# Performance work log

Measured on AMD Instinct MI355X. Metric: run time of the kernel, lower is better.

## Reference

```python
import jax, jax.numpy as jnp
import numpy as np


def _conv(x, w, stride):
    # Conv2d(k=3, stride, padding=1, bias=False), NCHW/OIHW
    return jax.lax.conv_general_dilated(
        x, w, (stride, stride), ((1, 1), (1, 1)),
        dimension_numbers=('NCHW', 'OIHW', 'NCHW'))


def _bn_silu(x, g, b, m, v):
    # BatchNorm2d (inference) + SiLU, fused elementwise
    scale = (g * jax.lax.rsqrt(v + 1e-5))[None, :, None, None]
    y = (x - m[None, :, None, None]) * scale + b[None, :, None, None]
    return y * jax.nn.sigmoid(y)


def _ss2d(x, in_w, dt_w, dt_b, B_w, C_w, A_log, D, out_w):
    # Low-rank 2D selective scan over flattened spatial tokens.
    Bn, C, H, W = x.shape
    L = H * W
    xt = x.reshape(Bn, C, L).transpose(0, 2, 1)            # [B,L,C]
    u = jnp.einsum('blc,rc->blr', xt, in_w)                # low-rank input [B,L,R]
    dt = jax.nn.softplus(jnp.einsum('blc,rc->blr', xt, dt_w) + dt_b)
    Bt = jnp.einsum('blc,nc->bln', xt, B_w)                # [B,L,N]
    Ct = jnp.einsum('blc,nc->bln', xt, C_w)                # [B,L,N]
    A = -jnp.exp(A_log)                                    # [R,N], stable (negative)

    def step(h, inp):
        u_t, dt_t, b_t, c_t = inp                          # [B,R],[B,R],[B,N],[B,N]
        dA = jnp.exp(dt_t[..., None] * A)                  # [B,R,N]
        h = dA * h + (dt_t[..., None] * b_t[:, None, :]) * u_t[..., None]
        y = jnp.einsum('brn,bn->br', h, c_t)               # [B,R]
        return h, (h, y)

    R, N = A_log.shape
    h0 = jnp.zeros((Bn, R, N), x.dtype)
    xs = (u.transpose(1, 0, 2), dt.transpose(1, 0, 2),
          Bt.transpose(1, 0, 2), Ct.transpose(1, 0, 2))
    _, (hs, ys) = jax.lax.scan(step, h0, xs)               # hs:[L,B,R,N] ys:[L,B,R]
    y = ys.transpose(1, 0, 2) + D * u                      # skip term D*u
    out = jnp.einsum('blr,cr->blc', y, out_w)              # project back to C
    x_out = (xt + out).transpose(0, 2, 1).reshape(Bn, C, H, W)
    state_seq = hs.transpose(1, 0, 2, 3)                   # [B,L,R,N]
    return x_out, state_seq


def setup_inputs() -> dict:
    key = jax.random.key(0)
    ks = jax.random.split(key, 24)
    f = jax.random.normal
    B, Cin, H, W = 8, 32, 112, 112
    E, R, N, NB = 64, 32, 64, 3
    inp = {}
    inp['x'] = f(ks[0], (B, Cin, H, W), jnp.float32)
    # stem
    inp['stem_w'] = f(ks[1], (E, Cin, 3, 3)) * 0.05
    inp['stem_g'] = 1.0 + 0.1 * f(ks[2], (E,))
    inp['stem_b'] = 0.1 * f(ks[3], (E,))
    inp['stem_m'] = 0.1 * f(ks[4], (E,))
    inp['stem_v'] = 1.0 + 0.1 * jax.random.uniform(ks[5], (E,))
    # SS2D blocks (stacked over num_blocks)
    inp['blk_in_w'] = f(ks[6], (NB, R, E)) * 0.1
    inp['blk_dt_w'] = f(ks[7], (NB, R, E)) * 0.05
    inp['blk_dt_b'] = f(ks[8], (NB, R)) * 0.1 - 2.0
    inp['blk_B_w'] = f(ks[9], (NB, N, E)) * 0.1
    inp['blk_C_w'] = f(ks[10], (NB, N, E)) * 0.1
    inp['blk_A_log'] = jnp.log(1.0 + jax.random.uniform(ks[11], (NB, R, N)) * 4.0)
    inp['blk_D'] = f(ks[12], (NB, R)) * 0.1
    inp['blk_out_w'] = f(ks[13], (NB, E, R)) * 0.1
    # down p4
    C4, C5 = 2 * E, 4 * E
    inp['p4_w'] = f(ks[14], (C4, E, 3, 3)) * 0.05
    inp['p4_g'] = 1.0 + 0.1 * f(ks[15], (C4,))
    inp['p4_b'] = 0.1 * f(ks[16], (C4,))
    inp['p4_m'] = 0.1 * f(ks[17], (C4,))
    inp['p4_v'] = 1.0 + 0.1 * jax.random.uniform(ks[18], (C4,))
    # down p5
    inp['p5_w'] = f(ks[19], (C5, C4, 3, 3)) * 0.05
    inp['p5_g'] = 1.0 + 0.1 * f(ks[20], (C5,))
    inp['p5_b'] = 0.1 * f(ks[21], (C5,))
    inp['p5_m'] = 0.1 * f(ks[22], (C5,))
    inp['p5_v'] = 1.0 + 0.1 * jax.random.uniform(ks[23], (C5,))
    return inp


def reference(x, stem_w, stem_g, stem_b, stem_m, stem_v,
              blk_in_w, blk_dt_w, blk_dt_b, blk_B_w, blk_C_w,
              blk_A_log, blk_D, blk_out_w,
              p4_w, p4_g, p4_b, p4_m, p4_v,
              p5_w, p5_g, p5_b, p5_m, p5_v):
    x = _bn_silu(_conv(x, stem_w, 2), stem_g, stem_b, stem_m, stem_v)
    states = []
    for i in range(blk_in_w.shape[0]):
        x, s = _ss2d(x, blk_in_w[i], blk_dt_w[i], blk_dt_b[i],
                     blk_B_w[i], blk_C_w[i], blk_A_log[i], blk_D[i], blk_out_w[i])
        states.append(s)
    p3 = x
    p4 = _bn_silu(_conv(p3, p4_w, 2), p4_g, p4_b, p4_m, p4_v)
    p5 = _bn_silu(_conv(p4, p5_w, 2), p5_g, p5_b, p5_m, p5_v)
    return (p3, p4, p5, jnp.stack(states))
```

## Files before the change

kernel.cpp:

```cpp
#include <hip/hip_runtime.h>
#include <cstdint>
#include <cstddef>

#define RFL(x) __builtin_amdgcn_readfirstlane(x)

constexpr int E  = 64;
constexpr int Rr = 32;
constexpr int Nn = 64;
constexpr int Lt = 3136;
constexpr int NC = 28;
constexpr int CL = 112;
constexpr int PD = 192;

__global__ __launch_bounds__(256) void k_wtrans(const float* __restrict__ in_w,
    const float* __restrict__ dt_w, const float* __restrict__ B_w,
    const float* __restrict__ C_w, float* __restrict__ wT) {
  int idx = blockIdx.x * 256 + threadIdx.x;
  if (idx >= 3 * 64 * PD) return;
  int o = idx % PD; int c = (idx / PD) & 63; int i = idx / (PD * 64);
  float v;
  if (o < 32)       v = in_w[(i * 32 + o) * 64 + c];
  else if (o < 64)  v = dt_w[(i * 32 + (o - 32)) * 64 + c];
  else if (o < 128) v = B_w[(i * 64 + (o - 64)) * 64 + c];
  else              v = C_w[(i * 64 + (o - 128)) * 64 + c];
  wT[idx] = v;
}

__global__ __launch_bounds__(256) void k_cwt2(const float* __restrict__ w,
    float* __restrict__ w3, int Cout, int Cin) {
  int idx = blockIdx.x * 256 + threadIdx.x;
  if (idx >= Cin * Cout * 9) return;
  int co = idx % Cout; int k = (idx / Cout) % 9; int ci = idx / (9 * Cout);
  w3[idx] = w[((size_t)co * Cin + ci) * 9 + k];
}

template<int CIN, int COUT, int HIN, int WIN>
__global__ __launch_bounds__(256) void k_conv(const float* __restrict__ x,
    const float* __restrict__ w3, const float* __restrict__ g, const float* __restrict__ bb,
    const float* __restrict__ m, const float* __restrict__ vv, float* __restrict__ out) {
  constexpr int HOUT = HIN / 2, WOUT = WIN / 2;
  constexpr int OWT = 7;
  constexpr int GWX = WOUT / OWT;
  constexpr int CIW = CIN / 4;
  __shared__ float xs[3][CIN][16];
  __shared__ float tbuf[4][64][8];

  int t = blockIdx.x;
  int b = t & 7; t >>= 3;
  int oh = t % HOUT; t /= HOUT;
  int gx = t % GWX; int cog = t / GWX;
  int lane = threadIdx.x & 63;
  int ws = RFL(threadIdx.x >> 6);
  int co = cog * 64 + lane;
  int iwb = gx * 14;
  int ih0 = oh * 2 - 1;

  for (int i = threadIdx.x; i < CIN * 3 * 16; i += 256) {
    int d = i & 15; int r3 = i >> 4;
    int kh = r3 / CIN; int ci = r3 & (CIN - 1);
    int iw = iwb + d - 1; int ih = ih0 + kh;
    float v = 0.f;
    if ((unsigned)iw < (unsigned)WIN && (unsigned)ih < (unsigned)HIN)
      v = x[(((size_t)(b * CIN + ci)) * HIN + ih) * WIN + iw];
    xs[kh][ci][d] = v;
  }
  __syncthreads();

  float acc[OWT];
#pragma unroll
  for (int o = 0; o < OWT; ++o) acc[o] = 0.f;

  int ci0 = ws * CIW;
#pragma unroll 2
  for (int cc = 0; cc < CIW; ++cc) {
    int ci = ci0 + cc;
    const float* wr = w3 + ((size_t)ci * 9) * COUT + co;
    float wk[9];
#pragma unroll
    for (int k = 0; k < 9; ++k) wk[k] = wr[(size_t)k * COUT];
#pragma unroll
    for (int kh = 0; kh < 3; ++kh) {
      const float4* tp4 = (const float4*)(&xs[kh][ci][0]);
      float4 q0 = tp4[0], q1 = tp4[1], q2 = tp4[2], q3 = tp4[3];
      float tp[16] = {q0.x, q0.y, q0.z, q0.w, q1.x, q1.y, q1.z, q1.w,
                      q2.x, q2.y, q2.z, q2.w, q3.x, q3.y, q3.z, q3.w};
#pragma unroll
      for (int o = 0; o < OWT; ++o) {
        acc[o] = fmaf(tp[2*o],     wk[kh*3+0], acc[o]);
        acc[o] = fmaf(tp[2*o + 1], wk[kh*3+1], acc[o]);
        acc[o] = fmaf(tp[2*o + 2], wk[kh*3+2], acc[o]);
      }
    }
  }
#pragma unroll
  for (int o = 0; o < OWT; ++o) tbuf[ws][lane][o] = acc[o];
  __syncthreads();

  for (int i = threadIdx.x; i < 64 * OWT; i += 256) {
    int cl = i / OWT, o = i - cl * OWT;
    float s = tbuf[0][cl][o] + tbuf[1][cl][o] + tbuf[2][cl][o] + tbuf[3][cl][o];
    int c2 = cog * 64 + cl;
    float scale = g[c2] * rsqrtf(vv[c2] + 1e-5f);
    float yv = (s - m[c2]) * scale + bb[c2];
    out[(((size_t)(b * COUT + c2)) * HOUT + oh) * WOUT + gx * OWT + o] =
        yv / (1.f + __expf(-yv));
  }
}

__global__ __launch_bounds__(256) void k_proj(const float* __restrict__ xin,
    const float* __restrict__ wT, const float* __restrict__ dt_b, float* __restrict__ P) {
  __shared__ float sm[64 * 196];
  int b = blockIdx.x & 7, tl = blockIdx.x >> 3;
  int l0 = tl * 64;
  int tid = threadIdx.x;
  for (int k = 0; k < 16; ++k) {
    int idx = k * 256 + tid; int c = idx >> 6, li = idx & 63;
    sm[c * 65 + li] = xin[(size_t)(b * 64 + c) * Lt + l0 + li];
  }
  __syncthreads();
  int tok = tid & 63;
  int og = RFL(tid >> 6);
  const float* wbase = wT + og * 48;
  float acc[48];
#pragma unroll
  for (int j = 0; j < 48; ++j) acc[j] = 0.f;
  for (int c = 0; c < 64; ++c) {
    float xv = sm[c * 65 + tok];
    const float4* w4 = (const float4*)(wbase + c * PD);
#pragma unroll
    for (int j = 0; j < 12; ++j) {
      float4 wv = __ldg(w4 + j);
      acc[4 * j + 0] = fmaf(xv, wv.x, acc[4 * j + 0]);
      acc[4 * j + 1] = fmaf(xv, wv.y, acc[4 * j + 1]);
      acc[4 * j + 2] = fmaf(xv, wv.z, acc[4 * j + 2]);
      acc[4 * j + 3] = fmaf(xv, wv.w, acc[4 * j + 3]);
    }
  }
  __syncthreads();
#pragma unroll
  for (int j = 0; j < 48; ++j) {
    int o = og * 48 + j;
    float v = acc[j];
    if (o >= 32 && o < 64) {
      v += dt_b[o - 32];
      v = fmaxf(v, 0.f) + log1pf(__expf(-fabsf(v)));
    }
    sm[tok * 196 + o] = v;
  }
  __syncthreads();
  float* dst = P + ((size_t)(b * Lt + l0)) * PD;
#pragma unroll
  for (int it = 0; it < 12; ++it) {
    int f = it * 1024 + tid * 4;
    int tk = f / 192;
    float4 v = *(const float4*)(&sm[tk * 196 + (f - tk * 192)]);
    *(float4*)(dst + f) = v;
  }
}

__global__ __launch_bounds__(256) void k_scan1(const float* __restrict__ P,
    const float* __restrict__ A_log, float* __restrict__ hfin, float* __restrict__ Pc) {
  __shared__ float xl[16][132];
  int bid = blockIdx.x;
  int b = bid & 7; int rest = bid >> 3;
  int c = rest % NC; int rg = rest / NC;
  int ws = RFL(threadIdx.x >> 6);
  int r = rg * 4 + ws;
  int n = threadIdx.x & 63;
  float a = -__expf(A_log[r * 64 + n]);
  const float* base = P + ((size_t)(b * Lt + c * CL)) * PD;
  int tl = threadIdx.x >> 4;
  int colb = (threadIdx.x & 15) * 8;
  float h = 0.f, sdt = 0.f;
  for (int s0 = 0; s0 < CL; s0 += 16) {
    __syncthreads();
    const float4* src = (const float4*)(base + (size_t)(s0 + tl) * PD + colb);
    float4 v0 = src[0], v1 = src[1];
    *(float4*)(&xl[tl][colb]) = v0;
    *(float4*)(&xl[tl][colb + 4]) = v1;
    __syncthreads();
#pragma unroll
    for (int tt = 0; tt < 16; ++tt) {
      float dt = xl[tt][32 + r];
      float u  = xl[tt][r];
      float bt = xl[tt][64 + n];
      h = fmaf(__expf(dt * a), h, (dt * u) * bt);
      sdt += dt;
    }
  }
  int o = ((b * 32 + r) * NC + c) * 64 + n;
  hfin[o] = h;
  Pc[o] = __expf(a * sdt);
}

__global__ __launch_bounds__(256) void k_scan2(const float* __restrict__ hfin,
    const float* __restrict__ Pc, float* __restrict__ Hs) {
  int wid = blockIdx.x * 4 + (threadIdx.x >> 6);
  int b = wid >> 5, r = wid & 31, n = threadIdx.x & 63;
  float H = 0.f;
  int base = ((b * 32 + r) * NC) * 64 + n;
#pragma unroll
  for (int c = 0; c < NC; ++c) {
    Hs[base + c * 64] = H;
    H = fmaf(Pc[base + c * 64], H, hfin[base + c * 64]);
  }
}

__global__ __launch_bounds__(256) void k_scan3(const float* __restrict__ P,
    const float* __restrict__ A_log, const float* __restrict__ Hs,
    const float* __restrict__ Dp, float* __restrict__ states, float* __restrict__ y) {
  __shared__ float xl[16][196];
  __shared__ __align__(16) float ylds[4][16][68];
  int bid = blockIdx.x;
  int b = bid & 7; int rest = bid >> 3;
  int c = rest % NC; int rg = rest / NC;
  int ws = RFL(threadIdx.x >> 6);
  int r = rg * 4 + ws;
  int n = threadIdx.x & 63;
  float a = -__expf(A_log[r * 64 + n]);
  float Dr = Dp[r];
  const float* base = P + ((size_t)(b * Lt + c * CL)) * PD;
  float h = Hs[((b * 32 + r) * NC + c) * 64 + n];
  float* st = states + ((size_t)(b * Lt + c * CL) * 32 + r) * 64 + n;
  float* yrow = y + (size_t)(b * 32 + r) * Lt + c * CL;
  int tl = threadIdx.x >> 4;
  int colb = (threadIdx.x & 15) * 12;
  for (int s0 = 0; s0 < CL; s0 += 16) {
    __syncthreads();
    const float4* src = (const float4*)(base + (size_t)(s0 + tl) * PD + colb);
    float4 v0 = src[0], v1 = src[1], v2 = src[2];
    *(float4*)(&xl[tl][colb])     = v0;
    *(float4*)(&xl[tl][colb + 4]) = v1;
    *(float4*)(&xl[tl][colb + 8]) = v2;
    __syncthreads();
#pragma unroll
    for (int tt = 0; tt < 16; ++tt) {
      float dt = xl[tt][32 + r];
      float u  = xl[tt][r];
      float bt = xl[tt][64 + n];
      float ct = xl[tt][128 + n];
      h = fmaf(__expf(dt * a), h, (dt * u) * bt);
      st[(size_t)(s0 + tt) * 2048] = h;
      ylds[ws][tt][n] = h * ct;
    }
    if (n < 16) {
      const float4* rp = (const float4*)(&ylds[ws][n][0]);
      float a0 = 0.f, a1 = 0.f, a2 = 0.f, a3 = 0.f;
#pragma unroll
      for (int k = 0; k < 16; ++k) {
        float4 pv = rp[k];
        a0 += pv.x; a1 += pv.y; a2 += pv.z; a3 += pv.w;
      }
      float sum = (a0 + a1) + (a2 + a3);
      float uu = xl[n][r];
      yrow[s0 + n] = sum + Dr * uu;
    }
  }
}

__global__ __launch_bounds__(256) void k_outproj(const float* __restrict__ xin,
    const float* __restrict__ y, const float* __restrict__ ow, float* __restrict__ xout) {
  __shared__ float ylds[32 * 64];
  int b = blockIdx.x & 7, tl = blockIdx.x >> 3;
  int l0 = tl * 64;
  int tid = threadIdx.x;
  for (int k = 0; k < 8; ++k) {
    int idx = k * 256 + tid; int r = idx >> 6, li = idx & 63;
    ylds[r * 64 + li] = y[(size_t)(b * 32 + r) * Lt + l0 + li];
  }
  __syncthreads();
  int li = tid & 63, cg = RFL(tid >> 6);
  for (int cc = 0; cc < 16; ++cc) {
    int ci = cg * 16 + cc;
    float acc = xin[(size_t)(b * 64 + ci) * Lt + l0 + li];
    const float4* w4 = (const float4*)(ow + ci * 32);
#pragma unroll
    for (int r4 = 0; r4 < 8; ++r4) {
      float4 wv = __ldg(w4 + r4);
      acc = fmaf(ylds[(r4 * 4 + 0) * 64 + li], wv.x, acc);
      acc = fmaf(ylds[(r4 * 4 + 1) * 64 + li], wv.y, acc);
      acc = fmaf(ylds[(r4 * 4 + 2) * 64 + li], wv.z, acc);
      acc = fmaf(ylds[(r4 * 4 + 3) * 64 + li], wv.w, acc);
    }
    xout[(size_t)(b * 64 + ci) * Lt + l0 + li] = acc;
  }
}

extern "C" void kernel_launch(void* const* d_in, const int* in_sizes, int n_in,
                              void* d_out, int out_size, void* d_ws, size_t ws_size,
                              hipStream_t stream) {
  const float* x      = (const float*)d_in[0];
  const float* stem_w = (const float*)d_in[1];
  const float* stem_g = (const float*)d_in[2];
  const float* stem_b = (const float*)d_in[3];
  const float* stem_m = (const float*)d_in[4];
  const float* stem_v = (const float*)d_in[5];
  const float* in_w   = (const float*)d_in[6];
  const float* dt_w   = (const float*)d_in[7];
  const float* dt_b   = (const float*)d_in[8];
  const float* B_w    = (const float*)d_in[9];
  const float* C_w    = (const float*)d_in[10];
  const float* A_log  = (const float*)d_in[11];
  const float* Dp     = (const float*)d_in[12];
  const float* out_w  = (const float*)d_in[13];
  const float* p4_w   = (const float*)d_in[14];
  const float* p4_g   = (const float*)d_in[15];
  const float* p4_b   = (const float*)d_in[16];
  const float* p4_m   = (const float*)d_in[17];
  const float* p4_v   = (const float*)d_in[18];
  const float* p5_w   = (const float*)d_in[19];
  const float* p5_g   = (const float*)d_in[20];
  const float* p5_b   = (const float*)d_in[21];
  const float* p5_m   = (const float*)d_in[22];
  const float* p5_v   = (const float*)d_in[23];

  float* out = (float*)d_out;
  float* wsf = (float*)d_ws;

  float* p3out = out;
  float* p4out = out + 1605632;
  float* p5out = out + 2408448;
  float* stout = out + 2809856;

  float* x0    = wsf;
  float* x1    = wsf + 1605632;
  float* Pb    = wsf + 3211264;
  float* yb    = wsf + 8028160;
  float* hfin  = wsf + 8830976;
  float* Pc    = wsf + 9289728;
  float* Hs    = wsf + 9748480;
  float* wT    = wsf + 10207232;
  float* w3s   = wsf + 10244096;
  float* w34   = wsf + 10262528;
  float* w35   = wsf + 10336256;

  k_wtrans<<<144, 256, 0, stream>>>(in_w, dt_w, B_w, C_w, wT);
  k_cwt2<<<72, 256, 0, stream>>>(stem_w, w3s, 64, 32);
  k_cwt2<<<288, 256, 0, stream>>>(p4_w, w34, 128, 64);
  k_cwt2<<<1152, 256, 0, stream>>>(p5_w, w35, 256, 128);

  k_conv<32, 64, 112, 112><<<3584, 256, 0, stream>>>(
      x, w3s, stem_g, stem_b, stem_m, stem_v, x0);

  const float* xi = x0;
  for (int i = 0; i < 3; ++i) {
    k_proj<<<392, 256, 0, stream>>>(xi, wT + i * 64 * PD, dt_b + i * 32, Pb);
    k_scan1<<<1792, 256, 0, stream>>>(Pb, A_log + i * 2048, hfin, Pc);
    k_scan2<<<64, 256, 0, stream>>>(hfin, Pc, Hs);
    k_scan3<<<1792, 256, 0, stream>>>(Pb, A_log + i * 2048, Hs, Dp + i * 32,
                                      stout + (size_t)i * 51380224, yb);
    float* dst = (i == 2) ? p3out : ((i == 0) ? x1 : x0);
    k_outproj<<<392, 256, 0, stream>>>(xi, yb, out_w + i * 2048, dst);
    xi = dst;
  }

  k_conv<64, 128, 56, 56><<<1792, 256, 0, stream>>>(
      p3out, w34, p4_g, p4_b, p4_m, p4_v, p4out);
  k_conv<128, 256, 28, 28><<<896, 256, 0, stream>>>(
      p4out, w35, p5_g, p5_b, p5_m, p5_v, p5out);
}
```

Before: 427.0 us.

## Split scan into state-writer and y-reducer kernels, rechunk to 32x98

The fused scan kernel is split into two kernels. One is a 1024-thread-per-block kernel that recomputes the recurrence for all 32 ranks of a chunk and writes the states tensor. Because each token's 2048 contiguous state floats are written by a single block, the stores are more coalesced. The other kernel recomputes the recurrence only to produce y. Chunking changes from 28x112 to 32x98 tokens with 14-token tiles, and the x1 buffer is placed in not-yet-written output memory (the third block's state slot). The cost is that the recurrence is computed twice and P is read from global memory an extra time.

```diff
diff --git a/kernel.cpp b/kernel.cpp
--- a/kernel.cpp
+++ b/kernel.cpp
@@ -8,8 +8,9 @@
 constexpr int Rr = 32;
 constexpr int Nn = 64;
 constexpr int Lt = 3136;
-constexpr int NC = 28;
-constexpr int CL = 112;
+constexpr int NC = 32;
+constexpr int CL = 98;
+constexpr int TT = 14;
 constexpr int PD = 192;
 
 __global__ __launch_bounds__(256) void k_wtrans(const float* __restrict__ in_w,
@@ -160,27 +161,25 @@
 
 __global__ __launch_bounds__(256) void k_scan1(const float* __restrict__ P,
     const float* __restrict__ A_log, float* __restrict__ hfin, float* __restrict__ Pc) {
-  __shared__ float xl[16][132];
+  __shared__ float xl[TT][132];
   int bid = blockIdx.x;
   int b = bid & 7; int rest = bid >> 3;
-  int c = rest % NC; int rg = rest / NC;
+  int c = rest & 31; int rg = rest >> 5;
   int ws = RFL(threadIdx.x >> 6);
   int r = rg * 4 + ws;
   int n = threadIdx.x & 63;
   float a = -__expf(A_log[r * 64 + n]);
   const float* base = P + ((size_t)(b * Lt + c * CL)) * PD;
-  int tl = threadIdx.x >> 4;
-  int colb = (threadIdx.x & 15) * 8;
   float h = 0.f, sdt = 0.f;
-  for (int s0 = 0; s0 < CL; s0 += 16) {
-    __syncthreads();
-    const float4* src = (const float4*)(base + (size_t)(s0 + tl) * PD + colb);
-    float4 v0 = src[0], v1 = src[1];
-    *(float4*)(&xl[tl][colb]) = v0;
-    *(float4*)(&xl[tl][colb + 4]) = v1;
-    __syncthreads();
-#pragma unroll
-    for (int tt = 0; tt < 16; ++tt) {
+  for (int s0 = 0; s0 < CL; s0 += TT) {
+    __syncthreads();
+    for (int j = threadIdx.x; j < TT * 32; j += 256) {
+      int tl = j >> 5, c4 = (j & 31) * 4;
+      *(float4*)(&xl[tl][c4]) = *(const float4*)(base + (size_t)(s0 + tl) * PD + c4);
+    }
+    __syncthreads();
+#pragma unroll
+    for (int tt = 0; tt < TT; ++tt) {
       float dt = xl[tt][32 + r];
       float u  = xl[tt][r];
       float bt = xl[tt][64 + n];
@@ -206,14 +205,50 @@
   }
 }
 
-__global__ __launch_bounds__(256) void k_scan3(const float* __restrict__ P,
+__global__ __launch_bounds__(1024) void k_scanst(const float* __restrict__ P,
     const float* __restrict__ A_log, const float* __restrict__ Hs,
-    const float* __restrict__ Dp, float* __restrict__ states, float* __restrict__ y) {
-  __shared__ float xl[16][196];
-  __shared__ __align__(16) float ylds[4][16][68];
+    float* __restrict__ states) {
+  __shared__ float xl[TT][132];
+  int bid = blockIdx.x;
+  int b = bid & 7; int c = bid >> 3;
+  int tid = threadIdx.x;
+  int ws = RFL(tid >> 6);
+  int n = tid & 63;
+  float a0 = -__expf(A_log[ws * 64 + n]);
+  float a1 = -__expf(A_log[(ws + 16) * 64 + n]);
+  float h0 = Hs[((b * 32 + ws) * NC + c) * 64 + n];
+  float h1 = Hs[((b * 32 + ws + 16) * NC + c) * 64 + n];
+  const float* base = P + ((size_t)(b * Lt + c * CL)) * PD;
+  float* stb = states + ((size_t)(b * Lt + c * CL)) * 2048 + n;
+  for (int s0 = 0; s0 < CL; s0 += TT) {
+    __syncthreads();
+    for (int j = tid; j < TT * 32; j += 1024) {
+      int tl = j >> 5, c4 = (j & 31) * 4;
+      *(float4*)(&xl[tl][c4]) = *(const float4*)(base + (size_t)(s0 + tl) * PD + c4);
+    }
+    __syncthreads();
+#pragma unroll
+    for (int tt = 0; tt < TT; ++tt) {
+      float bt = xl[tt][64 + n];
+      float dt0 = xl[tt][32 + ws],      u0 = xl[tt][ws];
+      float dt1 = xl[tt][32 + ws + 16], u1 = xl[tt][ws + 16];
+      h0 = fmaf(__expf(dt0 * a0), h0, (dt0 * u0) * bt);
+      h1 = fmaf(__expf(dt1 * a1), h1, (dt1 * u1) * bt);
+      float* sto = stb + (size_t)(s0 + tt) * 2048;
+      sto[ws * 64] = h0;
+      sto[(ws + 16) * 64] = h1;
+    }
+  }
+}
+
+__global__ __launch_bounds__(256) void k_scany(const float* __restrict__ P,
+    const float* __restrict__ A_log, const float* __restrict__ Hs,
+    const float* __restrict__ Dp, float* __restrict__ y) {
+  __shared__ float xl[TT][196];
+  __shared__ __align__(16) float ylds[4][TT][68];
   int bid = blockIdx.x;
   int b = bid & 7; int rest = bid >> 3;
-  int c = rest % NC; int rg = rest / NC;
+  int c = rest & 31; int rg = rest >> 5;
   int ws = RFL(threadIdx.x >> 6);
   int r = rg * 4 + ws;
   int n = threadIdx.x & 63;
@@ -221,29 +256,24 @@
   float Dr = Dp[r];
   const float* base = P + ((size_t)(b * Lt + c * CL)) * PD;
   float h = Hs[((b * 32 + r) * NC + c) * 64 + n];
-  float* st = states + ((size_t)(b * Lt + c * CL) * 32 + r) * 64 + n;
   float* yrow = y + (size_t)(b * 32 + r) * Lt + c * CL;
-  int tl = threadIdx.x >> 4;
-  int colb = (threadIdx.x & 15) * 12;
-  for (int s0 = 0; s0 < CL; s0 += 16) {
-    __syncthreads();
-    const float4* src = (const float4*)(base + (size_t)(s0 + tl) * PD + colb);
-    float4 v0 = src[0], v1 = src[1], v2 = src[2];
-    *(float4*)(&xl[tl][colb])     = v0;
-    *(float4*)(&xl[tl][colb + 4]) = v1;
-    *(float4*)(&xl[tl][colb + 8]) = v2;
-    __syncthreads();
-#pragma unroll
-    for (int tt = 0; tt < 16; ++tt) {
+  for (int s0 = 0; s0 < CL; s0 += TT) {
+    __syncthreads();
+    for (int j = threadIdx.x; j < TT * 48; j += 256) {
+      int tl = j / 48, c4 = (j - tl * 48) * 4;
+      *(float4*)(&xl[tl][c4]) = *(const float4*)(base + (size_t)(s0 + tl) * PD + c4);
+    }
+    __syncthreads();
+#pragma unroll
+    for (int tt = 0; tt < TT; ++tt) {
       float dt = xl[tt][32 + r];
       float u  = xl[tt][r];
       float bt = xl[tt][64 + n];
       float ct = xl[tt][128 + n];
       h = fmaf(__expf(dt * a), h, (dt * u) * bt);
-      st[(size_t)(s0 + tt) * 2048] = h;
       ylds[ws][tt][n] = h * ct;
     }
-    if (n < 16) {
+    if (n < TT) {
       const float4* rp = (const float4*)(&ylds[ws][n][0]);
       float a0 = 0.f, a1 = 0.f, a2 = 0.f, a3 = 0.f;
 #pragma unroll
@@ -322,17 +352,18 @@
   float* p5out = out + 2408448;
   float* stout = out + 2809856;
 
+  float* x1 = stout + (size_t)2 * 51380224;
+
   float* x0    = wsf;
-  float* x1    = wsf + 1605632;
-  float* Pb    = wsf + 3211264;
-  float* yb    = wsf + 8028160;
-  float* hfin  = wsf + 8830976;
-  float* Pc    = wsf + 9289728;
-  float* Hs    = wsf + 9748480;
-  float* wT    = wsf + 10207232;
-  float* w3s   = wsf + 10244096;
-  float* w34   = wsf + 10262528;
-  float* w35   = wsf + 10336256;
+  float* Pb    = wsf + 1605632;
+  float* yb    = wsf + 6422528;
+  float* hfin  = wsf + 7225344;
+  float* Pc    = wsf + 7749632;
+  float* Hs    = wsf + 8273920;
+  float* wT    = wsf + 8798208;
+  float* w3s   = wsf + 8835072;
+  float* w34   = wsf + 8853504;
+  float* w35   = wsf + 8927232;
 
   k_wtrans<<<144, 256, 0, stream>>>(in_w, dt_w, B_w, C_w, wT);
   k_cwt2<<<72, 256, 0, stream>>>(stem_w, w3s, 64, 32);
@@ -345,10 +376,11 @@
   const float* xi = x0;
   for (int i = 0; i < 3; ++i) {
     k_proj<<<392, 256, 0, stream>>>(xi, wT + i * 64 * PD, dt_b + i * 32, Pb);
-    k_scan1<<<1792, 256, 0, stream>>>(Pb, A_log + i * 2048, hfin, Pc);
+    k_scan1<<<2048, 256, 0, stream>>>(Pb, A_log + i * 2048, hfin, Pc);
     k_scan2<<<64, 256, 0, stream>>>(hfin, Pc, Hs);
-    k_scan3<<<1792, 256, 0, stream>>>(Pb, A_log + i * 2048, Hs, Dp + i * 32,
-                                      stout + (size_t)i * 51380224, yb);
+    k_scanst<<<256, 1024, 0, stream>>>(Pb, A_log + i * 2048, Hs,
+                                       stout + (size_t)i * 51380224);
+    k_scany<<<2048, 256, 0, stream>>>(Pb, A_log + i * 2048, Hs, Dp + i * 32, yb);
     float* dst = (i == 2) ? p3out : ((i == 0) ? x1 : x0);
     k_outproj<<<392, 256, 0, stream>>>(xi, yb, out_w + i * 2048, dst);
     xi = dst;
```

Result: slower. 534.6 us (+25.2%).
